# Kernel optimization log

Hardware: AMD Instinct MI355X
Metric: run time of the kernel (lower is better)

Reference implementation:

```python
import jax, jax.numpy as jnp
import numpy as np

N, C, E = 32768, 256, 16
LN_EPS = 1e-5
ENT_EPS = 1e-12


def setup_inputs() -> dict:
    key = jax.random.key(0)
    ks = jax.random.split(key, 8)
    return {
        "inputs": jax.random.normal(ks[0], (N, C), jnp.float32),
        "conv_out": jax.random.normal(ks[1], (N, C), jnp.float32),
        "domain_emb": jax.random.normal(ks[2], (C,), jnp.float32),
        "share_W": jax.random.normal(ks[3], (C, C), jnp.float32) * 0.02,
        "share_b": jnp.zeros((C,), jnp.float32),
        "gate_W": jax.random.normal(ks[4], (C, E), jnp.float32) * 0.1,
        "gate_b": jnp.zeros((E,), jnp.float32),
        "expert_W": jax.random.normal(ks[5], (E, C, C), jnp.float32) * 0.02,
        "expert_b": jnp.zeros((E, C), jnp.float32),
        "ln_gamma": jnp.ones((C,), jnp.float32),
        "ln_beta": jnp.zeros((C,), jnp.float32),
    }


def reference(inputs, conv_out, domain_emb, share_W, share_b, gate_W, gate_b,
              expert_W, expert_b, ln_gamma, ln_beta):
    n_exp = gate_W.shape[-1]

    # shared expert
    share_out = inputs @ share_W + share_b                      # (N, C)

    # LayerNorm on (stand-in) sparse-conv features + domain embedding
    mu = conv_out.mean(-1, keepdims=True)
    var = conv_out.var(-1, keepdims=True)
    route = (conv_out - mu) / jnp.sqrt(var + LN_EPS) * ln_gamma + ln_beta
    route = route + domain_emb                                   # (N, C)

    # router (eval path: no noise)
    gate_logits = route @ gate_W + gate_b                        # (N, E)
    w = jax.nn.softmax(gate_logits.astype(jnp.float32), axis=-1).astype(inputs.dtype)

    # entropy -> dynamic k per token
    entropy = -jnp.sum(w * jnp.log(w + ENT_EPS), axis=-1)        # (N,)
    max_entropy = jnp.log(jnp.float32(n_exp))
    k = jnp.ceil(1.0 + entropy / max_entropy * (n_exp - 1)).astype(jnp.int32)
    k = jnp.clip(k, 1, n_exp)                                    # (N,)

    # dynamic top-k selection mask (sort descending, keep first k)
    order = jnp.argsort(-w, axis=-1)                             # (N, E) descending ranks
    positions = jnp.arange(n_exp)[None, :]
    mask_sorted = positions < k[:, None]                         # (N, E) bool
    inv = jnp.argsort(order, axis=-1)                            # inverse permutation
    sel_mask = jnp.take_along_axis(mask_sorted, inv, axis=-1)    # (N, E) bool, expert-order
    combine = jnp.where(sel_mask, w, jnp.zeros_like(w))          # (N, E) combine weights

    # Switch-style load balancing loss
    frac_tokens = sel_mask.astype(jnp.float32).mean(0)           # (E,)
    frac_probs = w.astype(jnp.float32).mean(0)                   # (E,)
    loss_balance = jnp.mean(frac_tokens * frac_probs) * (n_exp ** 2)

    # expert compute + combine (dense, equivalent to gather/scatter loop)
    expert_out = jnp.einsum('nc,ecd->ned', inputs, expert_W) + expert_b  # (N, E, C)
    moe_out = jnp.einsum('ne,nec->nc', combine, expert_out)     # (N, C)

    return moe_out + share_out, loss_balance
```

## Files before the change

### kernel.cpp

```cpp
#include <hip/hip_runtime.h>
#include <hip/hip_bf16.h>

#define NTOK 32768
#define CH   256
#define NEXP 16

typedef __attribute__((ext_vector_type(8)))  short short8;
typedef __attribute__((ext_vector_type(16))) float f32x16;

#define MFMA32(a, b, c) __builtin_amdgcn_mfma_f32_32x32x16_bf16((a), (b), (c), 0, 0, 0)
#define BC8(v) __builtin_bit_cast(short8, (v))

#define GLD16(lds, g) __builtin_amdgcn_global_load_lds(                          \
    (const __attribute__((address_space(1))) unsigned int*)(g),                  \
    (__attribute__((address_space(3))) unsigned int*)(lds), 16, 0, 0)

static __device__ __forceinline__ unsigned short f2bf(float f) {
  unsigned int u = __builtin_bit_cast(unsigned int, f);
  unsigned int r = (u + 0x7fffu + ((u >> 16) & 1u)) >> 16;
  return (unsigned short)r;
}


__global__ __launch_bounds__(256) void wconvert_kernel(
    const float* __restrict__ share_W, const float* __restrict__ expert_W,
    uint4* __restrict__ wp) {
  int g = blockIdx.x * 256 + threadIdx.x;
  int e = g >> 13;
  int r = g & 8191;
  int lane = r & 63;
  int kb = (r >> 6) & 15;
  int db = r >> 10;
  int d  = db * 32 + (lane & 31);
  int k0 = kb * 16 + ((lane >> 5) << 3);
  const float* src = (e < 16) ? (expert_W + (size_t)e * 65536) : share_W;
  unsigned int p[4];
#pragma unroll
  for (int j = 0; j < 4; j++) {
    float f0 = src[(size_t)(k0 + 2 * j) * 256 + d];
    float f1 = src[(size_t)(k0 + 2 * j + 1) * 256 + d];
    p[j] = (unsigned int)f2bf(f0) | ((unsigned int)f2bf(f1) << 16);
  }
  wp[g] = make_uint4(p[0], p[1], p[2], p[3]);
}

__global__ __launch_bounds__(256) void gate_kernel(
    const float* __restrict__ inputs, const float* __restrict__ conv_out,
    const float* __restrict__ domain_emb, const float* __restrict__ gate_W,
    const float* __restrict__ gate_b, const float* __restrict__ ln_gamma,
    const float* __restrict__ ln_beta, uint4* __restrict__ apack,
    float* __restrict__ combine, float* __restrict__ frac_part) {
  __shared__ __align__(16) unsigned short atile[64 * 256];
  __shared__ __align__(16) float gwT[16 * 260];
  __shared__ float route[4][256];
  __shared__ float fred[2][4][16];
  int t = threadIdx.x, b = blockIdx.x;
  int w = t >> 6, l = t & 63;

  for (int i = 0; i < 16; i++) {
    int idx = i * 256 + t;
    gwT[(idx & 15) * 260 + (idx >> 4)] = gate_W[idx];
  }

  for (int i = 0; i < 8; i++) {
    int idx = i * 256 + t;
    int row = idx >> 5;
    int j = idx & 31;
    const float4* src = (const float4*)(inputs + ((size_t)b * 64 + row) * 256 + j * 8);
    float4 f0 = src[0], f1 = src[1];
    unsigned int p0 = (unsigned int)f2bf(f0.x) | ((unsigned int)f2bf(f0.y) << 16);
    unsigned int p1 = (unsigned int)f2bf(f0.z) | ((unsigned int)f2bf(f0.w) << 16);
    unsigned int p2 = (unsigned int)f2bf(f1.x) | ((unsigned int)f2bf(f1.y) << 16);
    unsigned int p3 = (unsigned int)f2bf(f1.z) | ((unsigned int)f2bf(f1.w) << 16);
    int s = j ^ (row & 31);
    *(uint4*)(atile + (row * 32 + s) * 8) = make_uint4(p0, p1, p2, p3);
  }
  __syncthreads();
  for (int i = 0; i < 8; i++) {
    int L = i * 256 + t;
    int ll = L & 63;
    int mb = (L >> 6) & 1, kb = L >> 7;
    int row = mb * 32 + (ll & 31);
    int j = kb * 2 + (ll >> 5);
    int s = j ^ (row & 31);
    apack[(size_t)b * 2048 + L] = *(const uint4*)(atile + (row * 32 + s) * 8);
  }

  int lc = l * 4;
  float4 g4 = *(const float4*)(ln_gamma + lc);
  float4 be4 = *(const float4*)(ln_beta + lc);
  float4 de4 = *(const float4*)(domain_emb + lc);
  int e = l & 15, q = l >> 4;
  float gb = gate_b[e];
  float psel = 0.f, pw = 0.f;

  int n0 = b * 64 + w * 16;
  float4 x = *(const float4*)(conv_out + (size_t)n0 * 256 + lc);
  for (int i = 0; i < 16; i++) {
    float4 xn = *(const float4*)(conv_out + (size_t)(n0 + ((i + 1) & 15)) * 256 + lc);

    float s1 = x.x + x.y + x.z + x.w;
#pragma unroll
    for (int off = 1; off < 64; off <<= 1) s1 += __shfl_xor(s1, off);
    float mu = s1 * (1.f / 256.f);
    float dx = x.x - mu, dy = x.y - mu, dz = x.z - mu, dw = x.w - mu;
    float s2 = dx * dx + dy * dy + dz * dz + dw * dw;
#pragma unroll
    for (int off = 1; off < 64; off <<= 1) s2 += __shfl_xor(s2, off);
    float rstd = rsqrtf(s2 * (1.f / 256.f) + 1e-5f);
    float4 r;
    r.x = dx * rstd * g4.x + be4.x + de4.x;
    r.y = dy * rstd * g4.y + be4.y + de4.y;
    r.z = dz * rstd * g4.z + be4.z + de4.z;
    r.w = dw * rstd * g4.w + be4.w + de4.w;
    *(float4*)(&route[w][lc]) = r;
    asm volatile("s_waitcnt lgkmcnt(0)" ::: "memory");
    __builtin_amdgcn_wave_barrier();

    float acc = 0.f;
#pragma unroll
    for (int ii = 0; ii < 16; ii++) {
      float4 r4 = *(const float4*)(&route[w][q * 64 + ii * 4]);
      float4 gv = *(const float4*)(&gwT[e * 260 + q * 64 + ii * 4]);
      acc += r4.x * gv.x + r4.y * gv.y + r4.z * gv.z + r4.w * gv.w;
    }
    acc += __shfl_xor(acc, 16);
    acc += __shfl_xor(acc, 32);
    float logit = acc + gb;

    float m = logit;
#pragma unroll
    for (int off = 1; off < 16; off <<= 1) m = fmaxf(m, __shfl_xor(m, off));
    float p = expf(logit - m);
    float sum = p;
#pragma unroll
    for (int off = 1; off < 16; off <<= 1) sum += __shfl_xor(sum, off);
    float wv = p / sum;

    float et = -wv * logf(wv + 1e-12f);
    float ent = et;
#pragma unroll
    for (int off = 1; off < 16; off <<= 1) ent += __shfl_xor(ent, off);
    float kf = ceilf(1.f + ent * (15.f / 2.7725887f));
    int k = (int)kf;
    k = max(1, min(16, k));

    int base = l & 48;
    int rank = 0;
#pragma unroll
    for (int j = 0; j < 16; j++) {
      float wj = __shfl(wv, base + j);
      rank += (wj > wv) || (wj == wv && j < e);
    }
    int sel = rank < k;
    float cmb = sel ? wv : 0.f;
    int n = n0 + i;
    if (l < 16) combine[(size_t)n * 16 + e] = cmb;
    psel += (float)sel;
    pw += wv;

    x = xn;
  }

  if (l < 16) { fred[0][w][l] = psel; fred[1][w][l] = pw; }
  __syncthreads();
  if (t < 32) {
    int kind = t >> 4, ee = t & 15;
    frac_part[b * 32 + t] = fred[kind][0][ee] + fred[kind][1][ee] +
                            fred[kind][2][ee] + fred[kind][3][ee];
  }
}

__global__ __launch_bounds__(512, 2) void moe_gemm_kernel(
    const uint4* __restrict__ apack, const uint4* __restrict__ wpack,
    const float* __restrict__ combine, const float* __restrict__ expert_b,
    const float* __restrict__ share_b, float* __restrict__ out) {
  extern __shared__ __align__(16) char smem[];
  uint4* atile  = (uint4*)smem;
  uint4* btile0 = (uint4*)(smem + 65536);
  uint4* btile1 = (uint4*)(smem + 98304);
  float* wtile  = (float*)(smem + 131072);

  int t = threadIdx.x, b = blockIdx.x;
  int w = t >> 6, l = t & 63;
  int mbp = w >> 2;
  int dbp = w & 3;

#pragma unroll
  for (int i = 0; i < 8; i++) {
    int g = w * 8 + i;
    int kb = g >> 2, mb = g & 3;
    const uint4* src = apack + ((size_t)(2 * b + (mb >> 1)) * 2048 + (size_t)(kb * 2 + (mb & 1)) * 64 + l);
    GLD16(atile + g * 64, src);
  }
#pragma unroll
  for (int i = 0; i < 4; i++) {
    int g = w * 4 + i;
    int kbl = g >> 3, db = g & 7;
    GLD16(btile0 + g * 64, wpack + ((size_t)db * 1024 + kbl * 64 + l));
  }
  {
    const float* cg = combine + (size_t)b * 2048;
#pragma unroll
    for (int i = 0; i < 4; i++) {
      int idx = i * 512 + t;
      wtile[(idx & 15) * 128 + (idx >> 4)] = cg[idx];
    }
  }

  f32x16 facc[2][2];
#pragma unroll
  for (int mi = 0; mi < 2; mi++)
#pragma unroll
    for (int d = 0; d < 2; d++)
#pragma unroll
      for (int r = 0; r < 16; r++) facc[mi][d][r] = 0.f;
  f32x16 zc;
#pragma unroll
  for (int r = 0; r < 16; r++) zc[r] = 0.f;

  short8 areg[2][4];
  f32x16 tacc[2][2];
  uint4* bufs[2] = {btile0, btile1};
  int rowoff = (l >> 5) * 4;

  for (int e = 0; e < 17; e++) {
#pragma unroll
    for (int q = 0; q < 4; q++) {
      int s = e * 4 + q;
      __syncthreads();

      if (s < 67) {
        int sn = s + 1;
        int en = sn >> 2, qn = sn & 3;
        uint4* nb = bufs[sn & 1];
#pragma unroll
        for (int i = 0; i < 4; i++) {
          int g = w * 4 + i;
          int kbl = g >> 3, db = g & 7;
          GLD16(nb + g * 64,
                wpack + ((size_t)en * 8192 + (size_t)db * 1024 + (qn * 4 + kbl) * 64 + l));
        }
      }

#pragma unroll
      for (int mi = 0; mi < 2; mi++)
#pragma unroll
        for (int kbl = 0; kbl < 4; kbl++)
          areg[mi][kbl] = BC8(atile[((size_t)(q * 4 + kbl) * 4 + (mbp * 2 + mi)) * 64 + l]);

      const uint4* cb = bufs[s & 1];
      if (q == 0) {
        {
          short8 b0 = BC8(cb[(size_t)(0 * 8 + dbp * 2 + 0) * 64 + l]);
          short8 b1 = BC8(cb[(size_t)(0 * 8 + dbp * 2 + 1) * 64 + l]);
          tacc[0][0] = MFMA32(areg[0][0], b0, zc);
          tacc[0][1] = MFMA32(areg[0][0], b1, zc);
          tacc[1][0] = MFMA32(areg[1][0], b0, zc);
          tacc[1][1] = MFMA32(areg[1][0], b1, zc);
        }
#pragma unroll
        for (int kbl = 1; kbl < 4; kbl++) {
          short8 b0 = BC8(cb[(size_t)(kbl * 8 + dbp * 2 + 0) * 64 + l]);
          short8 b1 = BC8(cb[(size_t)(kbl * 8 + dbp * 2 + 1) * 64 + l]);
          tacc[0][0] = MFMA32(areg[0][kbl], b0, tacc[0][0]);
          tacc[0][1] = MFMA32(areg[0][kbl], b1, tacc[0][1]);
          tacc[1][0] = MFMA32(areg[1][kbl], b0, tacc[1][0]);
          tacc[1][1] = MFMA32(areg[1][kbl], b1, tacc[1][1]);
        }
      } else {
#pragma unroll
        for (int kbl = 0; kbl < 4; kbl++) {
          short8 b0 = BC8(cb[(size_t)(kbl * 8 + dbp * 2 + 0) * 64 + l]);
          short8 b1 = BC8(cb[(size_t)(kbl * 8 + dbp * 2 + 1) * 64 + l]);
          tacc[0][0] = MFMA32(areg[0][kbl], b0, tacc[0][0]);
          tacc[0][1] = MFMA32(areg[0][kbl], b1, tacc[0][1]);
          tacc[1][0] = MFMA32(areg[1][kbl], b0, tacc[1][0]);
          tacc[1][1] = MFMA32(areg[1][kbl], b1, tacc[1][1]);
        }
      }

      if (q == 3) {
        if (e < 16) {
#pragma unroll
          for (int mi = 0; mi < 2; mi++)
#pragma unroll
            for (int rg = 0; rg < 4; rg++) {
              float4 w4 = *(const float4*)&wtile[e * 128 + (mbp * 2 + mi) * 32 + 8 * rg + rowoff];
              float wj[4] = {w4.x, w4.y, w4.z, w4.w};
#pragma unroll
              for (int j = 0; j < 4; j++) {
                facc[mi][0][rg * 4 + j] += wj[j] * tacc[mi][0][rg * 4 + j];
                facc[mi][1][rg * 4 + j] += wj[j] * tacc[mi][1][rg * 4 + j];
              }
            }
        } else {
#pragma unroll
          for (int mi = 0; mi < 2; mi++)
#pragma unroll
            for (int r = 0; r < 16; r++) {
              facc[mi][0][r] += tacc[mi][0][r];
              facc[mi][1][r] += tacc[mi][1][r];
            }
        }
      }
    }
  }

  int col = l & 31;
  int cg0 = (dbp * 2 + 0) * 32 + col;
  int cg1 = (dbp * 2 + 1) * 32 + col;
  float sb0 = share_b[cg0], sb1 = share_b[cg1];
  float eb0[16], eb1[16];
#pragma unroll
  for (int e2 = 0; e2 < 16; e2++) {
    eb0[e2] = expert_b[e2 * 256 + cg0];
    eb1[e2] = expert_b[e2 * 256 + cg1];
  }
#pragma unroll
  for (int e2 = 0; e2 < 16; e2++)
#pragma unroll
    for (int mi = 0; mi < 2; mi++)
#pragma unroll
      for (int rg = 0; rg < 4; rg++) {
        float4 w4 = *(const float4*)&wtile[e2 * 128 + (mbp * 2 + mi) * 32 + 8 * rg + rowoff];
        float wj[4] = {w4.x, w4.y, w4.z, w4.w};
#pragma unroll
        for (int j = 0; j < 4; j++) {
          facc[mi][0][rg * 4 + j] += wj[j] * eb0[e2];
          facc[mi][1][rg * 4 + j] += wj[j] * eb1[e2];
        }
      }
#pragma unroll
  for (int mi = 0; mi < 2; mi++)
#pragma unroll
    for (int r = 0; r < 16; r++) {
      int row = (mbp * 2 + mi) * 32 + (r & 3) + ((r >> 2) << 3) + rowoff;
      size_t n = (size_t)b * 128 + row;
      out[n * 256 + cg0] = facc[mi][0][r] + sb0;
      out[n * 256 + cg1] = facc[mi][1][r] + sb1;
    }
}

__global__ __launch_bounds__(256) void finalize_kernel(
    const float* __restrict__ frac_part, float* __restrict__ loss_out) {
  __shared__ float acc[8][32];
  int t = threadIdx.x;
  int col = t & 31, seg = t >> 5;
  float s = 0.f;
  for (int i = seg; i < 512; i += 8) s += frac_part[i * 32 + col];
  acc[seg][col] = s;
  __syncthreads();
  if (t < 32) {
    float v = 0.f;
#pragma unroll
    for (int sg = 0; sg < 8; sg++) v += acc[sg][t];
    acc[0][t] = v;
  }
  __syncthreads();
  if (t == 0) {
    float loss = 0.f;
    for (int e = 0; e < 16; e++) {
      float ft = acc[0][e] * (1.f / 32768.f);
      float fp = acc[0][16 + e] * (1.f / 32768.f);
      loss += ft * fp;
    }
    loss_out[0] = loss * 16.f;
  }
}

extern "C" void kernel_launch(void* const* d_in, const int* in_sizes, int n_in,
                              void* d_out, int out_size, void* d_ws, size_t ws_size,
                              hipStream_t stream) {
  const float* inputs   = (const float*)d_in[0];
  const float* conv_out = (const float*)d_in[1];
  const float* demb     = (const float*)d_in[2];
  const float* share_W  = (const float*)d_in[3];
  const float* share_b  = (const float*)d_in[4];
  const float* gate_W   = (const float*)d_in[5];
  const float* gate_b   = (const float*)d_in[6];
  const float* expert_W = (const float*)d_in[7];
  const float* expert_b = (const float*)d_in[8];
  const float* ln_g     = (const float*)d_in[9];
  const float* ln_b     = (const float*)d_in[10];
  float* out = (float*)d_out;
  char* ws = (char*)d_ws;

  uint4* apack   = (uint4*)(ws);
  uint4* wpack   = (uint4*)(ws + 16777216);
  float* combine = (float*)(ws + 19005440);
  float* frac    = (float*)(ws + 21102592);

  hipFuncSetAttribute((const void*)moe_gemm_kernel,
                      hipFuncAttributeMaxDynamicSharedMemorySize, 139264);

  wconvert_kernel<<<dim3(544), dim3(256), 0, stream>>>(share_W, expert_W, wpack);
  gate_kernel<<<dim3(512), dim3(256), 0, stream>>>(inputs, conv_out, demb, gate_W,
                                                   gate_b, ln_g, ln_b, apack, combine, frac);
  moe_gemm_kernel<<<dim3(256), dim3(512), 139264, stream>>>(apack, wpack, combine,
                                                            expert_b, share_b, out);
  finalize_kernel<<<dim3(1), dim3(256), 0, stream>>>(frac, out + 8388608);
}
```

Before: 243.3 us.

## Widen gate kernel to 512 threads and split GEMM barrier with partial vmcnt waits

The gate kernel now launches 512 threads per block, so each wave handles 8 tokens instead of 16. Each lane caches its gate weights in registers, and the dot product uses four independent accumulators. In the MoE GEMM, the single __syncthreads per stage becomes two s_barriers around a partial vmcnt(4) wait, which lets the next weight prefetch stay in flight while the current buffer is confirmed. It also raises wave priority around the MFMA block. Together these target latency and synchronization stalls, but they bring extra register pressure in the gate kernel and depend on exact vmcnt bookkeeping for correctness.

```diff
diff --git a/kernel.cpp b/kernel.cpp
--- a/kernel.cpp
+++ b/kernel.cpp
@@ -44,7 +44,7 @@
   wp[g] = make_uint4(p[0], p[1], p[2], p[3]);
 }
 
-__global__ __launch_bounds__(256) void gate_kernel(
+__global__ __launch_bounds__(512, 2) void gate_kernel(
     const float* __restrict__ inputs, const float* __restrict__ conv_out,
     const float* __restrict__ domain_emb, const float* __restrict__ gate_W,
     const float* __restrict__ gate_b, const float* __restrict__ ln_gamma,
@@ -52,18 +52,18 @@
     float* __restrict__ combine, float* __restrict__ frac_part) {
   __shared__ __align__(16) unsigned short atile[64 * 256];
   __shared__ __align__(16) float gwT[16 * 260];
-  __shared__ float route[4][256];
-  __shared__ float fred[2][4][16];
+  __shared__ float route[8][256];
+  __shared__ float fred[2][8][16];
   int t = threadIdx.x, b = blockIdx.x;
   int w = t >> 6, l = t & 63;
 
-  for (int i = 0; i < 16; i++) {
-    int idx = i * 256 + t;
+  for (int i = 0; i < 8; i++) {
+    int idx = i * 512 + t;
     gwT[(idx & 15) * 260 + (idx >> 4)] = gate_W[idx];
   }
 
-  for (int i = 0; i < 8; i++) {
-    int idx = i * 256 + t;
+  for (int i = 0; i < 4; i++) {
+    int idx = i * 512 + t;
     int row = idx >> 5;
     int j = idx & 31;
     const float4* src = (const float4*)(inputs + ((size_t)b * 64 + row) * 256 + j * 8);
@@ -76,8 +76,8 @@
     *(uint4*)(atile + (row * 32 + s) * 8) = make_uint4(p0, p1, p2, p3);
   }
   __syncthreads();
-  for (int i = 0; i < 8; i++) {
-    int L = i * 256 + t;
+  for (int i = 0; i < 4; i++) {
+    int L = i * 512 + t;
     int ll = L & 63;
     int mb = (L >> 6) & 1, kb = L >> 7;
     int row = mb * 32 + (ll & 31);
@@ -94,10 +94,15 @@
   float gb = gate_b[e];
   float psel = 0.f, pw = 0.f;
 
-  int n0 = b * 64 + w * 16;
+  float4 gwreg[16];
+#pragma unroll
+  for (int ii = 0; ii < 16; ii++)
+    gwreg[ii] = *(const float4*)&gwT[e * 260 + q * 64 + ii * 4];
+
+  int n0 = b * 64 + w * 8;
   float4 x = *(const float4*)(conv_out + (size_t)n0 * 256 + lc);
-  for (int i = 0; i < 16; i++) {
-    float4 xn = *(const float4*)(conv_out + (size_t)(n0 + ((i + 1) & 15)) * 256 + lc);
+  for (int i = 0; i < 8; i++) {
+    float4 xn = *(const float4*)(conv_out + (size_t)(n0 + ((i + 1) & 7)) * 256 + lc);
 
     float s1 = x.x + x.y + x.z + x.w;
 #pragma unroll
@@ -117,13 +122,19 @@
     asm volatile("s_waitcnt lgkmcnt(0)" ::: "memory");
     __builtin_amdgcn_wave_barrier();
 
-    float acc = 0.f;
-#pragma unroll
-    for (int ii = 0; ii < 16; ii++) {
-      float4 r4 = *(const float4*)(&route[w][q * 64 + ii * 4]);
-      float4 gv = *(const float4*)(&gwT[e * 260 + q * 64 + ii * 4]);
-      acc += r4.x * gv.x + r4.y * gv.y + r4.z * gv.z + r4.w * gv.w;
-    }
+    float a0 = 0.f, a1 = 0.f, a2 = 0.f, a3 = 0.f;
+#pragma unroll
+    for (int ii = 0; ii < 16; ii += 4) {
+      float4 r0 = *(const float4*)(&route[w][q * 64 + (ii + 0) * 4]);
+      float4 r1 = *(const float4*)(&route[w][q * 64 + (ii + 1) * 4]);
+      float4 r2 = *(const float4*)(&route[w][q * 64 + (ii + 2) * 4]);
+      float4 r3 = *(const float4*)(&route[w][q * 64 + (ii + 3) * 4]);
+      a0 += r0.x * gwreg[ii + 0].x + r0.y * gwreg[ii + 0].y + r0.z * gwreg[ii + 0].z + r0.w * gwreg[ii + 0].w;
+      a1 += r1.x * gwreg[ii + 1].x + r1.y * gwreg[ii + 1].y + r1.z * gwreg[ii + 1].z + r1.w * gwreg[ii + 1].w;
+      a2 += r2.x * gwreg[ii + 2].x + r2.y * gwreg[ii + 2].y + r2.z * gwreg[ii + 2].z + r2.w * gwreg[ii + 2].w;
+      a3 += r3.x * gwreg[ii + 3].x + r3.y * gwreg[ii + 3].y + r3.z * gwreg[ii + 3].z + r3.w * gwreg[ii + 3].w;
+    }
+    float acc = (a0 + a1) + (a2 + a3);
     acc += __shfl_xor(acc, 16);
     acc += __shfl_xor(acc, 32);
     float logit = acc + gb;
@@ -166,8 +177,10 @@
   __syncthreads();
   if (t < 32) {
     int kind = t >> 4, ee = t & 15;
-    frac_part[b * 32 + t] = fred[kind][0][ee] + fred[kind][1][ee] +
-                            fred[kind][2][ee] + fred[kind][3][ee];
+    float v = 0.f;
+#pragma unroll
+    for (int ww = 0; ww < 8; ww++) v += fred[kind][ww][ee];
+    frac_part[b * 32 + t] = v;
   }
 }
 
@@ -207,6 +220,7 @@
       wtile[(idx & 15) * 128 + (idx >> 4)] = cg[idx];
     }
   }
+  asm volatile("s_waitcnt lgkmcnt(0)" ::: "memory");
 
   f32x16 facc[2][2];
 #pragma unroll
@@ -228,7 +242,9 @@
 #pragma unroll
     for (int q = 0; q < 4; q++) {
       int s = e * 4 + q;
-      __syncthreads();
+
+      asm volatile("" ::: "memory");
+      __builtin_amdgcn_s_barrier();
 
       if (s < 67) {
         int sn = s + 1;
@@ -241,7 +257,13 @@
           GLD16(nb + g * 64,
                 wpack + ((size_t)en * 8192 + (size_t)db * 1024 + (qn * 4 + kbl) * 64 + l));
         }
+        asm volatile("s_waitcnt vmcnt(4)" ::: "memory");
+      } else {
+        asm volatile("s_waitcnt vmcnt(0)" ::: "memory");
       }
+
+      __builtin_amdgcn_s_barrier();
+      asm volatile("" ::: "memory");
 
 #pragma unroll
       for (int mi = 0; mi < 2; mi++)
@@ -250,6 +272,7 @@
           areg[mi][kbl] = BC8(atile[((size_t)(q * 4 + kbl) * 4 + (mbp * 2 + mi)) * 64 + l]);
 
       const uint4* cb = bufs[s & 1];
+      __builtin_amdgcn_s_setprio(1);
       if (q == 0) {
         {
           short8 b0 = BC8(cb[(size_t)(0 * 8 + dbp * 2 + 0) * 64 + l]);
@@ -279,6 +302,7 @@
           tacc[1][1] = MFMA32(areg[1][kbl], b1, tacc[1][1]);
         }
       }
+      __builtin_amdgcn_s_setprio(0);
 
       if (q == 3) {
         if (e < 16) {
@@ -395,7 +419,7 @@
                       hipFuncAttributeMaxDynamicSharedMemorySize, 139264);
 
   wconvert_kernel<<<dim3(544), dim3(256), 0, stream>>>(share_W, expert_W, wpack);
-  gate_kernel<<<dim3(512), dim3(256), 0, stream>>>(inputs, conv_out, demb, gate_W,
+  gate_kernel<<<dim3(512), dim3(512), 0, stream>>>(inputs, conv_out, demb, gate_W,
                                                    gate_b, ln_g, ln_b, apack, combine, frac);
   moe_gemm_kernel<<<dim3(256), dim3(512), 139264, stream>>>(apack, wpack, combine,
                                                             expert_b, share_b, out);
```

Result: no change. 244.6 us (+0.5%).
